# Optimization experiments

Hardware: AMD Instinct MI355X
Metric: run time of the kernel (lower is better)

The kernel has to match this reference:

```python
import jax, jax.numpy as jnp
import numpy as np

N_NODES = 100000
N_EDGES = 1000000
D = 128          # input_dim == hidden_dim (required: h = zeros_like(nh) accumulates src_nf)
OUT = 128
NUM_TYPES = 5


def setup_inputs() -> dict:
    key = jax.random.key(0)
    ks = jax.random.split(key, 7)
    nh = jax.random.normal(ks[0], (N_NODES, D), dtype=jnp.float32)
    edge_y = jax.random.randint(ks[1], (N_EDGES,), 0, NUM_TYPES, dtype=jnp.int64)
    edge_index = jax.random.randint(ks[2], (2, N_EDGES), 0, N_NODES, dtype=jnp.int64)
    # nn.Linear weights, scaled for numerical sanity
    W_nf = jax.random.normal(ks[3], (D, D), dtype=jnp.float32) * 0.08
    W_attn = jax.random.normal(ks[4], (1, 2 * D), dtype=jnp.float32) * 0.08
    W_out = jax.random.normal(ks[5], (OUT, 2 * D), dtype=jnp.float32) * 0.08
    b_out = jax.random.normal(ks[6], (OUT,), dtype=jnp.float32) * 0.01
    return {"nh": nh, "edge_y": edge_y, "edge_index": edge_index,
            "W_nf": W_nf, "W_attn": W_attn, "W_out": W_out, "b_out": b_out}


def reference(nh, edge_y, edge_index, W_nf, W_attn, W_out, b_out):
    n = nh.shape[0]
    src, dst = edge_index[0], edge_index[1]

    # nf_lin applied once per node, then gathered per edge (same math as
    # self.nf_lin(nh[src]) since Linear is per-row)
    nfl = nh @ W_nf.T                                  # [N, D]
    src_nf = nfl[src]                                  # [E, D]
    dst_nf = nfl[dst]                                  # [E, D]

    # attn(cat([src_nf, dst_nf])) == src_nf @ a_src + dst_nf @ a_dst
    a_src, a_dst = W_attn[0, :D], W_attn[0, D:]
    ef = src_nf @ a_src + dst_nf @ a_dst               # [E]
    ef = jnp.where(ef >= 0, ef, 0.2 * ef)              # LeakyReLU(0.2)

    # scatter_softmax per (edge_type, dst) group: the per-type loop with
    # scatter_softmax over dst is exactly a segment softmax over composite
    # segments seg = dst*5 + type; the summed per-type scatter_adds equal
    # one segment_sum over dst.
    seg = dst * NUM_TYPES + edge_y                     # [E]
    num_seg = n * NUM_TYPES
    m = jax.ops.segment_max(ef, seg, num_segments=num_seg)
    ex = jnp.exp(ef - m[seg])
    denom = jax.ops.segment_sum(ex, seg, num_segments=num_seg)
    alpha = ex / denom[seg]                            # [E]

    h = jax.ops.segment_sum(alpha[:, None] * src_nf, dst, num_segments=n)  # [N, D]

    nf = jnp.concatenate([nh, h], axis=-1) @ W_out.T + b_out
    return jax.nn.relu(nf)
```

## Files before the change

### kernel.cpp

```cpp
#include <hip/hip_runtime.h>

#define NTYPES 5
#define EPB 16384
#define BKSH 5
#define BKDST 32
#define CAP 1024

typedef _Float16 half8 __attribute__((ext_vector_type(8)));
typedef _Float16 half4v __attribute__((ext_vector_type(4)));
typedef float float4v __attribute__((ext_vector_type(4)));

__device__ __forceinline__ void stage_f32(
    _Float16* lds, const float* __restrict__ g, int rows, int stride4, int off4,
    int grow0, int nmax, int t)
{
  const float4* g4 = (const float4*)g;
  for (int i = t; i < rows * 32; i += 256) {
    int row = i >> 5, q = i & 31;
    float4 v = make_float4(0.f, 0.f, 0.f, 0.f);
    int gr = grow0 + row;
    if (gr < nmax) v = g4[(size_t)gr * stride4 + off4 + q];
    half4v hv = { (_Float16)v.x, (_Float16)v.y, (_Float16)v.z, (_Float16)v.w };
    int byte = row * 256 + ((q * 8) ^ ((row & 7) << 4));
    *(half4v*)((char*)lds + byte) = hv;
  }
}

__device__ __forceinline__ half8 frag_ld(const _Float16* lds, int row, int khw) {
  int byte = row * 256 + ((khw * 2) ^ ((row & 7) << 4));
  return *(const half8*)((const char*)lds + byte);
}

__device__ __forceinline__ half8 cvt8(float4 v0, float4 v1) {
  half8 a;
  a[0] = (_Float16)v0.x; a[1] = (_Float16)v0.y; a[2] = (_Float16)v0.z; a[3] = (_Float16)v0.w;
  a[4] = (_Float16)v1.x; a[5] = (_Float16)v1.y; a[6] = (_Float16)v1.z; a[7] = (_Float16)v1.w;
  return a;
}

__global__ __launch_bounds__(256) void k_gemm0(
    const float* __restrict__ nh, const float* __restrict__ Wnf,
    const float* __restrict__ Wattn,
    float* __restrict__ s_src, float* __restrict__ s_dst,
    _Float16* __restrict__ nfl, _Float16* __restrict__ nh16, int n)
{
  __shared__ _Float16 wh[128 * 128];
  const int t = threadIdx.x, lane = t & 63, wv = t >> 6;
  const int r16 = lane & 15, g = lane >> 4;
  stage_f32(wh, Wnf, 128, 32, 0, 0, 1 << 30, t);
  float asrc[8], adst[8];
  #pragma unroll
  for (int nf = 0; nf < 8; ++nf) {
    asrc[nf] = Wattn[nf * 16 + r16];
    adst[nf] = Wattn[128 + nf * 16 + r16];
  }
  __syncthreads();
  const int nchunk = (n + 63) >> 6;
  for (int c = blockIdx.x; c < nchunk; c += gridDim.x) {
    const int base = c << 6;
    const int arow = base + wv * 16 + r16;
    const bool ok = arow < n;
    const float4* nh4 = (const float4*)(nh + (size_t)arow * 128);
    float4 av[8];
    const float4 z = make_float4(0.f, 0.f, 0.f, 0.f);
    #pragma unroll
    for (int q = 0; q < 8; ++q) av[q] = ok ? nh4[q * 4 + g * 2 - (q & 1) * (g * 2) + 0] : z;
    #pragma unroll
    for (int s = 0; s < 4; ++s) {
      av[2 * s]     = ok ? nh4[s * 8 + g * 2]     : z;
      av[2 * s + 1] = ok ? nh4[s * 8 + g * 2 + 1] : z;
    }
    float4v acc[8];
    #pragma unroll
    for (int nf = 0; nf < 8; ++nf) acc[nf] = (float4v){0.f, 0.f, 0.f, 0.f};
    #pragma unroll
    for (int s = 0; s < 4; ++s) {
      half8 a = cvt8(av[2 * s], av[2 * s + 1]);
      if (ok) *(half8*)(nh16 + (size_t)arow * 128 + s * 32 + g * 8) = a;
      #pragma unroll
      for (int nf = 0; nf < 8; ++nf)
        acc[nf] = __builtin_amdgcn_mfma_f32_16x16x32_f16(a, frag_ld(wh, nf * 16 + r16, s * 32 + g * 8), acc[nf], 0, 0, 0);
    }
    #pragma unroll
    for (int rr = 0; rr < 4; ++rr) {
      int node = base + wv * 16 + g * 4 + rr;
      if (node >= n) continue;
      size_t ro = (size_t)node * 128;
      #pragma unroll
      for (int nf = 0; nf < 8; ++nf) nfl[ro + nf * 16 + r16] = (_Float16)acc[nf][rr];
    }
    float ss[4] = {0.f, 0.f, 0.f, 0.f}, sd[4] = {0.f, 0.f, 0.f, 0.f};
    #pragma unroll
    for (int nf = 0; nf < 8; ++nf)
      #pragma unroll
      for (int rr = 0; rr < 4; ++rr) {
        ss[rr] = fmaf(acc[nf][rr], asrc[nf], ss[rr]);
        sd[rr] = fmaf(acc[nf][rr], adst[nf], sd[rr]);
      }
    #pragma unroll
    for (int m = 1; m <= 8; m <<= 1)
      #pragma unroll
      for (int rr = 0; rr < 4; ++rr) {
        ss[rr] += __shfl_xor(ss[rr], m);
        sd[rr] += __shfl_xor(sd[rr], m);
      }
    if (r16 == 0) {
      #pragma unroll
      for (int rr = 0; rr < 4; ++rr) {
        int node = base + wv * 16 + g * 4 + rr;
        if (node < n) { s_src[node] = ss[rr]; s_dst[node] = sd[rr]; }
      }
    }
  }
}

__global__ __launch_bounds__(256) void k_hist(
    const int* __restrict__ dsts, int* __restrict__ cnt, int e, int nbk, int nblk)
{
  __shared__ int hist[4096];
  const int t = threadIdx.x, b = blockIdx.x;
  for (int k = t; k < nbk; k += 256) hist[k] = 0;
  __syncthreads();
  const int i0 = b * EPB;
  const int iend = min(i0 + EPB, e);
  for (int i = i0 + t; i < iend; i += 256)
    atomicAdd(&hist[dsts[i] >> BKSH], 1);
  __syncthreads();
  for (int k = t; k < nbk; k += 256) cnt[k * nblk + b] = hist[k];
}

__global__ __launch_bounds__(256) void k_scan1(
    const int* __restrict__ deg, int* __restrict__ base, int* __restrict__ bsum, int n)
{
  __shared__ int ws[4];
  int t = threadIdx.x;
  int g0 = blockIdx.x * 1024 + t * 4;
  int4 v = make_int4(0, 0, 0, 0);
  if (g0 + 3 < n) v = *(const int4*)(deg + g0);
  else {
    if (g0     < n) v.x = deg[g0];
    if (g0 + 1 < n) v.y = deg[g0 + 1];
    if (g0 + 2 < n) v.z = deg[g0 + 2];
    if (g0 + 3 < n) v.w = deg[g0 + 3];
  }
  int s = v.x + v.y + v.z + v.w;
  int inc = s;
  #pragma unroll
  for (int d = 1; d < 64; d <<= 1) {
    int o = __shfl_up(inc, d);
    if ((t & 63) >= d) inc += o;
  }
  int wid = t >> 6;
  if ((t & 63) == 63) ws[wid] = inc;
  __syncthreads();
  int woff = 0;
  for (int w = 0; w < wid; ++w) woff += ws[w];
  int exc = woff + inc - s;
  if (g0 + 3 < n) {
    *(int4*)(base + g0) = make_int4(exc, exc + v.x, exc + v.x + v.y, exc + v.x + v.y + v.z);
  } else {
    if (g0     < n) base[g0]     = exc;
    if (g0 + 1 < n) base[g0 + 1] = exc + v.x;
    if (g0 + 2 < n) base[g0 + 2] = exc + v.x + v.y;
  }
  if (t == 255) bsum[blockIdx.x] = woff + inc;
}

__global__ __launch_bounds__(256) void k_scan2(
    const int* __restrict__ bsum, int* __restrict__ boff, int nb)
{
  __shared__ int ws[4];
  int t = threadIdx.x;
  int x = t < nb ? bsum[t] : 0;
  int inc = x;
  #pragma unroll
  for (int d = 1; d < 64; d <<= 1) {
    int o = __shfl_up(inc, d);
    if ((t & 63) >= d) inc += o;
  }
  int wid = t >> 6;
  if ((t & 63) == 63) ws[wid] = inc;
  __syncthreads();
  int woff = 0;
  for (int w = 0; w < wid; ++w) woff += ws[w];
  if (t < nb) boff[t] = woff + inc - x;
}

__global__ __launch_bounds__(256) void k_scan3(
    int* __restrict__ base, const int* __restrict__ boff, int n)
{
  int i = blockIdx.x * 256 + threadIdx.x;
  if (i < n) base[i] += boff[i >> 10];
}

__global__ __launch_bounds__(256) void k_scatter2(
    const int* __restrict__ ei, const int* __restrict__ ey,
    const int* __restrict__ cnt_s, unsigned* __restrict__ rec,
    int e, int nbk, int nblk)
{
  __shared__ int cur[4096];
  const int t = threadIdx.x, b = blockIdx.x;
  for (int k = t; k < nbk; k += 256) cur[k] = cnt_s[k * nblk + b];
  __syncthreads();
  const int i0 = b * EPB;
  const int iend = min(i0 + EPB, e);
  for (int i = i0 + t; i < iend; i += 256) {
    int s = ei[i], d = ei[e + i], ty = ey[i];
    int pos = atomicAdd(&cur[d >> BKSH], 1);
    rec[pos] = (unsigned)s | ((unsigned)ty << 17) | ((unsigned)(d & (BKDST - 1)) << 20);
  }
}

__global__ __launch_bounds__(256) void k_agg2(
    const unsigned* __restrict__ rec, const int* __restrict__ cnt_s,
    const float* __restrict__ s_src, const float* __restrict__ s_dst,
    const _Float16* __restrict__ nfl, _Float16* __restrict__ h,
    int n, int e, int nbk, int nblk)
{
  __shared__ unsigned ord[CAP];
  __shared__ float efl[CAP];
  __shared__ int dcnt[BKDST];
  __shared__ int dbase[BKDST + 1];
  __shared__ float sdl[BKDST];
  const int t = threadIdx.x;
  const int k = blockIdx.x;
  const int d0 = k << BKSH;
  const int ndst = min(BKDST, n - d0);
  const int bs = cnt_s[k * nblk];
  const int be = (k + 1 < nbk) ? cnt_s[(k + 1) * nblk] : e;
  const int cnt = be - bs;
  if (t < BKDST) {
    dcnt[t] = 0;
    if (t < ndst) sdl[t] = s_dst[d0 + t];
  }
  __syncthreads();
  const int g = t >> 4, l = t & 15;

  if (cnt <= CAP) {
    for (int i = t; i < cnt; i += 256)
      atomicAdd(&dcnt[(rec[bs + i] >> 20) & (BKDST - 1)], 1);
    __syncthreads();
    if (t < BKDST) {
      int v = dcnt[t];
      int inc = v;
      #pragma unroll
      for (int dd = 1; dd < BKDST; dd <<= 1) {
        int o = __shfl_up(inc, dd);
        if (t >= dd) inc += o;
      }
      dbase[t] = inc - v;
      dcnt[t]  = inc - v;
      if (t == BKDST - 1) dbase[BKDST] = inc;
    }
    __syncthreads();
    for (int i = t; i < cnt; i += 256) {
      unsigned p = rec[bs + i];
      int pos = atomicAdd(&dcnt[(p >> 20) & (BKDST - 1)], 1);
      ord[pos] = p;
    }
    __syncthreads();
    for (int i = t; i < cnt; i += 256) {
      unsigned p = ord[i];
      float ef = s_src[p & 0x1FFFF] + sdl[(p >> 20) & (BKDST - 1)];
      efl[i] = ef >= 0.f ? ef : 0.2f * ef;
    }
    __syncthreads();
    for (int di = g; di < ndst; di += 16) {
      int s0 = dbase[di], deg = dbase[di + 1] - s0;
      float acc[8] = {0.f, 0.f, 0.f, 0.f, 0.f, 0.f, 0.f, 0.f};
      if (deg > 0) {
        float mx[NTYPES];
        #pragma unroll
        for (int tt = 0; tt < NTYPES; ++tt) mx[tt] = -1e30f;
        for (int j0 = 0; j0 < deg; j0 += 16) {
          int jj = j0 + l;
          bool ok = jj < deg;
          float ef = ok ? efl[s0 + jj] : -1e30f;
          int ty = ok ? (int)((ord[s0 + jj] >> 17) & 7) : 7;
          #pragma unroll
          for (int tt = 0; tt < NTYPES; ++tt) {
            float v = (ty == tt) ? ef : -1e30f;
            v = fmaxf(v, __shfl_xor(v, 1)); v = fmaxf(v, __shfl_xor(v, 2));
            v = fmaxf(v, __shfl_xor(v, 4)); v = fmaxf(v, __shfl_xor(v, 8));
            mx[tt] = fmaxf(mx[tt], v);
          }
        }
        float sm[NTYPES];
        #pragma unroll
        for (int tt = 0; tt < NTYPES; ++tt) sm[tt] = 0.f;
        for (int j0 = 0; j0 < deg; j0 += 16) {
          int jj = j0 + l;
          bool ok = jj < deg;
          int ty = ok ? (int)((ord[s0 + jj] >> 17) & 7) : 7;
          float ex = ok ? __expf(efl[s0 + jj] - mx[ty]) : 0.f;
          if (ok) efl[s0 + jj] = ex;
          #pragma unroll
          for (int tt = 0; tt < NTYPES; ++tt) {
            float v = (ty == tt) ? ex : 0.f;
            v += __shfl_xor(v, 1); v += __shfl_xor(v, 2);
            v += __shfl_xor(v, 4); v += __shfl_xor(v, 8);
            sm[tt] += v;
          }
        }
        float rsm[NTYPES];
        #pragma unroll
        for (int tt = 0; tt < NTYPES; ++tt) rsm[tt] = sm[tt] > 0.f ? 1.f / sm[tt] : 0.f;
        int j = 0;
        for (; j + 4 <= deg; j += 4) {
          unsigned p0 = ord[s0 + j],     p1 = ord[s0 + j + 1];
          unsigned p2 = ord[s0 + j + 2], p3 = ord[s0 + j + 3];
          float a0 = efl[s0 + j]     * rsm[(p0 >> 17) & 7];
          float a1 = efl[s0 + j + 1] * rsm[(p1 >> 17) & 7];
          float a2 = efl[s0 + j + 2] * rsm[(p2 >> 17) & 7];
          float a3 = efl[s0 + j + 3] * rsm[(p3 >> 17) & 7];
          half8 x0 = *(const half8*)(nfl + (size_t)(p0 & 0x1FFFF) * 128 + l * 8);
          half8 x1 = *(const half8*)(nfl + (size_t)(p1 & 0x1FFFF) * 128 + l * 8);
          half8 x2 = *(const half8*)(nfl + (size_t)(p2 & 0x1FFFF) * 128 + l * 8);
          half8 x3 = *(const half8*)(nfl + (size_t)(p3 & 0x1FFFF) * 128 + l * 8);
          #pragma unroll
          for (int kk = 0; kk < 8; ++kk) acc[kk] = fmaf(a0, (float)x0[kk], acc[kk]);
          #pragma unroll
          for (int kk = 0; kk < 8; ++kk) acc[kk] = fmaf(a1, (float)x1[kk], acc[kk]);
          #pragma unroll
          for (int kk = 0; kk < 8; ++kk) acc[kk] = fmaf(a2, (float)x2[kk], acc[kk]);
          #pragma unroll
          for (int kk = 0; kk < 8; ++kk) acc[kk] = fmaf(a3, (float)x3[kk], acc[kk]);
        }
        for (; j < deg; ++j) {
          unsigned p0 = ord[s0 + j];
          float a0 = efl[s0 + j] * rsm[(p0 >> 17) & 7];
          half8 x0 = *(const half8*)(nfl + (size_t)(p0 & 0x1FFFF) * 128 + l * 8);
          #pragma unroll
          for (int kk = 0; kk < 8; ++kk) acc[kk] = fmaf(a0, (float)x0[kk], acc[kk]);
        }
      }
      half8 hv;
      #pragma unroll
      for (int kk = 0; kk < 8; ++kk) hv[kk] = (_Float16)acc[kk];
      *(half8*)(h + (size_t)(d0 + di) * 128 + l * 8) = hv;
    }
  } else {
    const int gb = (t & 63) & 48;
    for (int di = g; di < ndst; di += 16) {
      float mx[NTYPES], sm[NTYPES];
      #pragma unroll
      for (int tt = 0; tt < NTYPES; ++tt) { mx[tt] = -1e30f; sm[tt] = 0.f; }
      for (int j0 = 0; j0 < cnt; j0 += 16) {
        int jj = j0 + l;
        unsigned p = (jj < cnt) ? rec[bs + jj] : 0xFFFFFFFFu;
        bool mine = (p != 0xFFFFFFFFu) && (int)((p >> 20) & (BKDST - 1)) == di;
        float ef = -1e30f; int ty = 7;
        if (mine) {
          ef = s_src[p & 0x1FFFF] + sdl[di];
          ef = ef >= 0.f ? ef : 0.2f * ef;
          ty = (p >> 17) & 7;
        }
        #pragma unroll
        for (int tt = 0; tt < NTYPES; ++tt) {
          float v = (mine && ty == tt) ? ef : -1e30f;
          v = fmaxf(v, __shfl_xor(v, 1)); v = fmaxf(v, __shfl_xor(v, 2));
          v = fmaxf(v, __shfl_xor(v, 4)); v = fmaxf(v, __shfl_xor(v, 8));
          mx[tt] = fmaxf(mx[tt], v);
        }
      }
      for (int j0 = 0; j0 < cnt; j0 += 16) {
        int jj = j0 + l;
        unsigned p = (jj < cnt) ? rec[bs + jj] : 0xFFFFFFFFu;
        bool mine = (p != 0xFFFFFFFFu) && (int)((p >> 20) & (BKDST - 1)) == di;
        float ex = 0.f; int ty = 7;
        if (mine) {
          float ef = s_src[p & 0x1FFFF] + sdl[di];
          ef = ef >= 0.f ? ef : 0.2f * ef;
          ty = (p >> 17) & 7;
          ex = __expf(ef - mx[ty]);
        }
        #pragma unroll
        for (int tt = 0; tt < NTYPES; ++tt) {
          float v = (ty == tt) ? ex : 0.f;
          v += __shfl_xor(v, 1); v += __shfl_xor(v, 2);
          v += __shfl_xor(v, 4); v += __shfl_xor(v, 8);
          sm[tt] += v;
        }
      }
      float rsm[NTYPES];
      #pragma unroll
      for (int tt = 0; tt < NTYPES; ++tt) rsm[tt] = sm[tt] > 0.f ? 1.f / sm[tt] : 0.f;
      float acc[8] = {0.f, 0.f, 0.f, 0.f, 0.f, 0.f, 0.f, 0.f};
      for (int j0 = 0; j0 < cnt; j0 += 16) {
        int jj = j0 + l;
        unsigned p = (jj < cnt) ? rec[bs + jj] : 0xFFFFFFFFu;
        bool mine = (p != 0xFFFFFFFFu) && (int)((p >> 20) & (BKDST - 1)) == di;
        float al = 0.f;
        if (mine) {
          float ef = s_src[p & 0x1FFFF] + sdl[di];
          ef = ef >= 0.f ? ef : 0.2f * ef;
          int ty = (p >> 17) & 7;
          al = __expf(ef - mx[ty]) * rsm[ty];
        }
        unsigned pv = mine ? p : 0xFFFFFFFFu;
        for (int jj2 = 0; jj2 < 16; ++jj2) {
          unsigned pp = __shfl(pv, gb + jj2);
          float aa = __shfl(al, gb + jj2);
          if (pp != 0xFFFFFFFFu) {
            half8 x = *(const half8*)(nfl + (size_t)(pp & 0x1FFFF) * 128 + l * 8);
            #pragma unroll
            for (int kk = 0; kk < 8; ++kk) acc[kk] = fmaf(aa, (float)x[kk], acc[kk]);
          }
        }
      }
      half8 hv;
      #pragma unroll
      for (int kk = 0; kk < 8; ++kk) hv[kk] = (_Float16)acc[kk];
      *(half8*)(h + (size_t)(d0 + di) * 128 + l * 8) = hv;
    }
  }
}

__global__ __launch_bounds__(256) void k_gemmO(
    const _Float16* __restrict__ nh16, const _Float16* __restrict__ hbuf,
    const float* __restrict__ Wout, const float* __restrict__ bias,
    float* __restrict__ out, int n)
{
  __shared__ _Float16 w1[64 * 128], w2[64 * 128];
  const int t = threadIdx.x, lane = t & 63, wv = t >> 6;
  const int r16 = lane & 15, g = lane >> 4;
  const int jhalf = blockIdx.x & 1;
  stage_f32(w1, Wout, 64, 64, 0,  jhalf * 64, 1 << 30, t);
  stage_f32(w2, Wout, 64, 64, 32, jhalf * 64, 1 << 30, t);
  float bv[4];
  #pragma unroll
  for (int nf = 0; nf < 4; ++nf) bv[nf] = bias[jhalf * 64 + nf * 16 + r16];
  __syncthreads();
  const int nchunk = (n + 63) >> 6;
  const int gstride = gridDim.x >> 1;
  int c = blockIdx.x >> 1;
  half8 c1[4], c2[4];
  if (c < nchunk) {
    int arow = (c << 6) + wv * 16 + r16;
    bool ok = arow < n;
    #pragma unroll
    for (int s = 0; s < 4; ++s) {
      c1[s] = ok ? *(const half8*)(nh16 + (size_t)arow * 128 + s * 32 + g * 8) : (half8){};
      c2[s] = ok ? *(const half8*)(hbuf + (size_t)arow * 128 + s * 32 + g * 8) : (half8){};
    }
  }
  for (; c < nchunk; c += gstride) {
    const int base = c << 6;
    int cn = c + gstride;
    half8 n1[4] = {}, n2[4] = {};
    if (cn < nchunk) {
      int arow = (cn << 6) + wv * 16 + r16;
      bool ok = arow < n;
      #pragma unroll
      for (int s = 0; s < 4; ++s) {
        n1[s] = ok ? *(const half8*)(nh16 + (size_t)arow * 128 + s * 32 + g * 8) : (half8){};
        n2[s] = ok ? *(const half8*)(hbuf + (size_t)arow * 128 + s * 32 + g * 8) : (half8){};
      }
    }
    float4v acc[4];
    #pragma unroll
    for (int nf = 0; nf < 4; ++nf) acc[nf] = (float4v){0.f, 0.f, 0.f, 0.f};
    #pragma unroll
    for (int s = 0; s < 4; ++s) {
      #pragma unroll
      for (int nf = 0; nf < 4; ++nf) {
        acc[nf] = __builtin_amdgcn_mfma_f32_16x16x32_f16(c1[s], frag_ld(w1, nf * 16 + r16, s * 32 + g * 8), acc[nf], 0, 0, 0);
        acc[nf] = __builtin_amdgcn_mfma_f32_16x16x32_f16(c2[s], frag_ld(w2, nf * 16 + r16, s * 32 + g * 8), acc[nf], 0, 0, 0);
      }
    }
    #pragma unroll
    for (int rr = 0; rr < 4; ++rr) {
      int node = base + wv * 16 + g * 4 + rr;
      if (node >= n) continue;
      #pragma unroll
      for (int nf = 0; nf < 4; ++nf)
        out[(size_t)node * 128 + jhalf * 64 + nf * 16 + r16] = fmaxf(acc[nf][rr] + bv[nf], 0.f);
    }
    #pragma unroll
    for (int s = 0; s < 4; ++s) { c1[s] = n1[s]; c2[s] = n2[s]; }
  }
}

extern "C" void kernel_launch(void* const* d_in, const int* in_sizes, int n_in,
                              void* d_out, int out_size, void* d_ws, size_t ws_size,
                              hipStream_t stream) {
  const float* nh     = (const float*)d_in[0];
  const int*   edge_y = (const int*)d_in[1];
  const int*   ei     = (const int*)d_in[2];
  const float* W_nf   = (const float*)d_in[3];
  const float* W_attn = (const float*)d_in[4];
  const float* W_out  = (const float*)d_in[5];
  const float* b_out  = (const float*)d_in[6];
  float* out = (float*)d_out;
  const int n = in_sizes[0] / 128;
  const int e = in_sizes[1];
  const int nbk  = (n + BKDST - 1) >> BKSH;
  const int nblk = (e + EPB - 1) / EPB;
  const int ncnt = nbk * nblk;
  const int nb2  = (ncnt + 1023) / 1024;

  _Float16* nfl_h = (_Float16*)d_ws;
  _Float16* nh16  = nfl_h + (size_t)n * 128;
  _Float16* h_h   = nh16 + (size_t)n * 128;
  float* s_src = (float*)(h_h + (size_t)n * 128);
  float* s_dst = s_src + n;
  int*   cnt   = (int*)(s_dst + n);
  int*   bsum  = cnt + ncnt;
  int*   boff  = bsum + 256;
  unsigned* rec = (unsigned*)(boff + 256);

  k_gemm0<<<1280, 256, 0, stream>>>(nh, W_nf, W_attn, s_src, s_dst, nfl_h, nh16, n);
  k_hist<<<nblk, 256, 0, stream>>>(ei + e, cnt, e, nbk, nblk);
  k_scan1<<<nb2, 256, 0, stream>>>(cnt, cnt, bsum, ncnt);
  k_scan2<<<1, 256, 0, stream>>>(bsum, boff, nb2);
  k_scan3<<<(ncnt + 255) / 256, 256, 0, stream>>>(cnt, boff, ncnt);
  k_scatter2<<<nblk, 256, 0, stream>>>(ei, edge_y, cnt, rec, e, nbk, nblk);
  k_agg2<<<nbk, 256, 0, stream>>>(rec, cnt, s_src, s_dst, nfl_h, h_h, n, e, nbk, nblk);
  k_gemmO<<<1280, 256, 0, stream>>>(nh16, h_h, W_out, b_out, out, n);
}
```

Measured before the change: 181.4 us.

## Use coarser 128-dst buckets with 32-dst sub-blocks in aggregation

Bucketing now uses 128 destinations per bucket and 4096 edges per histogram block, so the histogram and scatter kernels keep a smaller shared array and there are more, smaller scatter blocks. The aggregation kernel still processes 32 destinations per block, but each block scans its whole 128-dst bucket and filters records for its sub-range. This cuts the number of buckets and the size of the count/scan matrix, at the cost of each aggregation block reading about four times as many records. A redundant preload loop in the first GEMM is also removed.

```diff
diff --git a/kernel.cpp b/kernel.cpp
--- a/kernel.cpp
+++ b/kernel.cpp
@@ -1,9 +1,10 @@
 #include <hip/hip_runtime.h>
 
 #define NTYPES 5
-#define EPB 16384
-#define BKSH 5
-#define BKDST 32
+#define EPB 4096
+#define BKSH 7
+#define BKDST 128
+#define SUBD 32
 #define CAP 1024
 
 typedef _Float16 half8 __attribute__((ext_vector_type(8)));
@@ -61,10 +62,8 @@
     const int arow = base + wv * 16 + r16;
     const bool ok = arow < n;
     const float4* nh4 = (const float4*)(nh + (size_t)arow * 128);
+    const float4 z = make_float4(0.f, 0.f, 0.f, 0.f);
     float4 av[8];
-    const float4 z = make_float4(0.f, 0.f, 0.f, 0.f);
-    #pragma unroll
-    for (int q = 0; q < 8; ++q) av[q] = ok ? nh4[q * 4 + g * 2 - (q & 1) * (g * 2) + 0] : z;
     #pragma unroll
     for (int s = 0; s < 4; ++s) {
       av[2 * s]     = ok ? nh4[s * 8 + g * 2]     : z;
@@ -117,7 +116,7 @@
 __global__ __launch_bounds__(256) void k_hist(
     const int* __restrict__ dsts, int* __restrict__ cnt, int e, int nbk, int nblk)
 {
-  __shared__ int hist[4096];
+  __shared__ int hist[1024];
   const int t = threadIdx.x, b = blockIdx.x;
   for (int k = t; k < nbk; k += 256) hist[k] = 0;
   __syncthreads();
@@ -198,7 +197,7 @@
     const int* __restrict__ cnt_s, unsigned* __restrict__ rec,
     int e, int nbk, int nblk)
 {
-  __shared__ int cur[4096];
+  __shared__ int cur[1024];
   const int t = threadIdx.x, b = blockIdx.x;
   for (int k = t; k < nbk; k += 256) cur[k] = cnt_s[k * nblk + b];
   __syncthreads();
@@ -219,49 +218,58 @@
 {
   __shared__ unsigned ord[CAP];
   __shared__ float efl[CAP];
-  __shared__ int dcnt[BKDST];
-  __shared__ int dbase[BKDST + 1];
-  __shared__ float sdl[BKDST];
+  __shared__ int dcnt[SUBD];
+  __shared__ int dbase[SUBD + 1];
+  __shared__ float sdl[SUBD];
   const int t = threadIdx.x;
-  const int k = blockIdx.x;
-  const int d0 = k << BKSH;
-  const int ndst = min(BKDST, n - d0);
+  const int sb = blockIdx.x;
+  const int d0 = sb << 5;
+  const int ndst = min(SUBD, n - d0);
+  const int k = sb >> 2;
+  const int sub = sb & 3;
   const int bs = cnt_s[k * nblk];
   const int be = (k + 1 < nbk) ? cnt_s[(k + 1) * nblk] : e;
   const int cnt = be - bs;
-  if (t < BKDST) {
+  if (t < SUBD) {
     dcnt[t] = 0;
     if (t < ndst) sdl[t] = s_dst[d0 + t];
   }
   __syncthreads();
   const int g = t >> 4, l = t & 15;
 
-  if (cnt <= CAP) {
-    for (int i = t; i < cnt; i += 256)
-      atomicAdd(&dcnt[(rec[bs + i] >> 20) & (BKDST - 1)], 1);
-    __syncthreads();
-    if (t < BKDST) {
-      int v = dcnt[t];
-      int inc = v;
-      #pragma unroll
-      for (int dd = 1; dd < BKDST; dd <<= 1) {
-        int o = __shfl_up(inc, dd);
-        if (t >= dd) inc += o;
-      }
-      dbase[t] = inc - v;
-      dcnt[t]  = inc - v;
-      if (t == BKDST - 1) dbase[BKDST] = inc;
-    }
-    __syncthreads();
+  for (int i = t; i < cnt; i += 256) {
+    int dl = (rec[bs + i] >> 20) & 127;
+    if ((dl >> 5) == sub) atomicAdd(&dcnt[dl & 31], 1);
+  }
+  __syncthreads();
+  if (t < SUBD) {
+    int v = dcnt[t];
+    int inc = v;
+    #pragma unroll
+    for (int dd = 1; dd < SUBD; dd <<= 1) {
+      int o = __shfl_up(inc, dd);
+      if (t >= dd) inc += o;
+    }
+    dbase[t] = inc - v;
+    dcnt[t]  = inc - v;
+    if (t == SUBD - 1) dbase[SUBD] = inc;
+  }
+  __syncthreads();
+  const int total = dbase[SUBD];
+
+  if (total <= CAP) {
     for (int i = t; i < cnt; i += 256) {
       unsigned p = rec[bs + i];
-      int pos = atomicAdd(&dcnt[(p >> 20) & (BKDST - 1)], 1);
-      ord[pos] = p;
+      int dl = (p >> 20) & 127;
+      if ((dl >> 5) == sub) {
+        int pos = atomicAdd(&dcnt[dl & 31], 1);
+        ord[pos] = p;
+      }
     }
     __syncthreads();
-    for (int i = t; i < cnt; i += 256) {
+    for (int i = t; i < total; i += 256) {
       unsigned p = ord[i];
-      float ef = s_src[p & 0x1FFFF] + sdl[(p >> 20) & (BKDST - 1)];
+      float ef = s_src[p & 0x1FFFF] + sdl[(p >> 20) & 31];
       efl[i] = ef >= 0.f ? ef : 0.2f * ef;
     }
     __syncthreads();
@@ -342,13 +350,14 @@
   } else {
     const int gb = (t & 63) & 48;
     for (int di = g; di < ndst; di += 16) {
+      const int want = sub * SUBD + di;
       float mx[NTYPES], sm[NTYPES];
       #pragma unroll
       for (int tt = 0; tt < NTYPES; ++tt) { mx[tt] = -1e30f; sm[tt] = 0.f; }
       for (int j0 = 0; j0 < cnt; j0 += 16) {
         int jj = j0 + l;
         unsigned p = (jj < cnt) ? rec[bs + jj] : 0xFFFFFFFFu;
-        bool mine = (p != 0xFFFFFFFFu) && (int)((p >> 20) & (BKDST - 1)) == di;
+        bool mine = (p != 0xFFFFFFFFu) && (int)((p >> 20) & 127) == want;
         float ef = -1e30f; int ty = 7;
         if (mine) {
           ef = s_src[p & 0x1FFFF] + sdl[di];
@@ -366,7 +375,7 @@
       for (int j0 = 0; j0 < cnt; j0 += 16) {
         int jj = j0 + l;
         unsigned p = (jj < cnt) ? rec[bs + jj] : 0xFFFFFFFFu;
-        bool mine = (p != 0xFFFFFFFFu) && (int)((p >> 20) & (BKDST - 1)) == di;
+        bool mine = (p != 0xFFFFFFFFu) && (int)((p >> 20) & 127) == want;
         float ex = 0.f; int ty = 7;
         if (mine) {
           float ef = s_src[p & 0x1FFFF] + sdl[di];
@@ -389,7 +398,7 @@
       for (int j0 = 0; j0 < cnt; j0 += 16) {
         int jj = j0 + l;
         unsigned p = (jj < cnt) ? rec[bs + jj] : 0xFFFFFFFFu;
-        bool mine = (p != 0xFFFFFFFFu) && (int)((p >> 20) & (BKDST - 1)) == di;
+        bool mine = (p != 0xFFFFFFFFu) && (int)((p >> 20) & 127) == want;
         float al = 0.f;
         if (mine) {
           float ef = s_src[p & 0x1FFFF] + sdl[di];
@@ -498,6 +507,7 @@
   const int nblk = (e + EPB - 1) / EPB;
   const int ncnt = nbk * nblk;
   const int nb2  = (ncnt + 1023) / 1024;
+  const int nsb  = (n + SUBD - 1) / SUBD;
 
   _Float16* nfl_h = (_Float16*)d_ws;
   _Float16* nh16  = nfl_h + (size_t)n * 128;
@@ -515,6 +525,6 @@
   k_scan2<<<1, 256, 0, stream>>>(bsum, boff, nb2);
   k_scan3<<<(ncnt + 255) / 256, 256, 0, stream>>>(cnt, boff, ncnt);
   k_scatter2<<<nblk, 256, 0, stream>>>(ei, edge_y, cnt, rec, e, nbk, nblk);
-  k_agg2<<<nbk, 256, 0, stream>>>(rec, cnt, s_src, s_dst, nfl_h, h_h, n, e, nbk, nblk);
+  k_agg2<<<nsb, 256, 0, stream>>>(rec, cnt, s_src, s_dst, nfl_h, h_h, n, e, nbk, nblk);
   k_gemmO<<<1280, 256, 0, stream>>>(nh16, h_h, W_out, b_out, out, n);
 }
```

New measurement: 165.4 us. 8.8% less time.
